# Kernel optimization log

Hardware: AMD Instinct MI355X
Metric: run time of the kernel (lower is better)

Reference implementation:

```python
import jax, jax.numpy as jnp
import numpy as np

TOP_K = 2
NUM_EXPERTS = 64
LOAD_BALANCE_ALPHA = 0.01
Z_LOSS_ALPHA = 1e-4
TEMPERATURE = 1.0  # buffer init, clamped to [0.1, 2.0] -> 1.0 (seq_len < 8192 branch)


def setup_inputs() -> dict:
    key = jax.random.key(0)
    k1, k2 = jax.random.split(key)
    x = jax.random.normal(k1, (4, 4096, 1024), dtype=jnp.float32)
    gate_w = jax.random.normal(k2, (NUM_EXPERTS, 1024), dtype=jnp.float32) * (1.0 / np.sqrt(1024))
    return {"x": x, "gate_w": gate_w}


def reference(x, gate_w):
    B, S, H = x.shape
    x_flat = x.reshape(-1, H)                      # [T, H], T = B*S
    logits = jnp.einsum('th,eh->te', x_flat, gate_w)  # [T, E]
    logits = logits / TEMPERATURE
    scores = jax.nn.softmax(logits, axis=-1)       # [T, E]
    # eval path: dynamic_top_k == top_k, no noise / capacity limitation
    top_scores, top_idx = jax.lax.top_k(scores, TOP_K)   # [T, K]
    top_scores = jax.nn.softmax(top_scores.astype(jnp.float32), axis=-1).astype(x.dtype)
    # load-balance loss: squared deviation of mean expert load from uniform
    expert_load = scores.mean(axis=0)              # [E]
    ideal = 1.0 / NUM_EXPERTS
    lb_loss = LOAD_BALANCE_ALPHA * NUM_EXPERTS * jnp.sum((expert_load - ideal) ** 2)
    # z-loss: mean squared logsumexp of gate logits
    z = jax.nn.logsumexp(logits, axis=-1)          # [T]
    z_loss = Z_LOSS_ALPHA * jnp.mean(z ** 2)
    total_loss = lb_loss + z_loss
    return top_scores, top_idx, total_loss
```

## Files before the change

kernel.cpp:

```cpp
#include <hip/hip_runtime.h>
#include <math.h>

#define T_TOK 16384
#define NEXP  64


__global__ void moe_prep(const float* __restrict__ gw, float* __restrict__ ws) {
    __shared__ float tile[64][65];
    const int b = blockIdx.x;
    const int tid = threadIdx.x;
    if (b == 0 && tid < 128) ws[tid] = 0.f;
#pragma unroll
    for (int it = 0; it < 16; ++it) {
        int idx = it * 256 + tid;
        int e = idx >> 6, kk = idx & 63;
        tile[e][kk] = gw[e * 1024 + b * 64 + kk];
    }
    __syncthreads();
#pragma unroll
    for (int it = 0; it < 16; ++it) {
        int idx = it * 256 + tid;
        int kk = idx >> 6, e = idx & 63;
        ws[128 + (b * 64 + kk) * 64 + e] = tile[e][kk];
    }
}

__device__ __forceinline__ void pstore(float* B, const float (&a)[8][8],
                                       int tg, int eg) {
#pragma unroll
    for (int i = 0; i < 8; ++i) {
        float* p = B + (tg + 8 * i) * 68 + (eg << 3);
        *(float4*)(p)     = make_float4(a[i][0], a[i][1], a[i][2], a[i][3]);
        *(float4*)(p + 4) = make_float4(a[i][4], a[i][5], a[i][6], a[i][7]);
    }
}
__device__ __forceinline__ void padd(float* B, const float (&a)[8][8],
                                     int tg, int eg) {
#pragma unroll
    for (int i = 0; i < 8; ++i) {
        float* p = B + (tg + 8 * i) * 68 + (eg << 3);
        float4 v0 = *(float4*)(p);
        float4 v1 = *(float4*)(p + 4);
        v0.x += a[i][0]; v0.y += a[i][1]; v0.z += a[i][2]; v0.w += a[i][3];
        v1.x += a[i][4]; v1.y += a[i][5]; v1.z += a[i][6]; v1.w += a[i][7];
        *(float4*)(p)     = v0;
        *(float4*)(p + 4) = v1;
    }
}

__launch_bounds__(1024, 4)
__global__ void moe_main(const float* __restrict__ x,
                         const float* __restrict__ wt,
                         float* __restrict__ acc_ws,
                         float* __restrict__ out) {
    __shared__ float xbuf[64 * 68];
    __shared__ float wbuf[64 * 68];
    __shared__ float sc[64 * 68];
    __shared__ float row_inv[64];
    __shared__ float colpart[16][64];
    __shared__ int   is_last;

    const int tid  = threadIdx.x;
    const int lane = tid & 63;
    const int wv   = __builtin_amdgcn_readfirstlane(tid >> 6);
    const int tg   = lane & 7;
    const int eg   = lane >> 3;
    const int tok0 = blockIdx.x << 6;

    const int rr = tid >> 4;
    const int cg = tid & 15;
    const float* gx = x + (((size_t)(tok0 + rr)) << 10) + (cg << 2);
    const float* gw = wt + (rr << 6) + (cg << 2);
    const int lof = rr * 68 + (cg << 2);

    float acc[8][8];
#pragma unroll
    for (int i = 0; i < 8; ++i)
#pragma unroll
        for (int j = 0; j < 8; ++j) acc[i][j] = 0.f;

    const float* xr = xbuf + tg * 68 + (wv << 2);
    const float* wr = wbuf + (wv * 4) * 68 + (eg << 3);

    float4 px = *(const float4*)gx;
    float4 pw = *(const float4*)gw;

#pragma unroll 1
    for (int s = 0; s < 16; ++s) {
        __syncthreads();
        *(float4*)(xbuf + lof) = px;
        *(float4*)(wbuf + lof) = pw;
        __syncthreads();
        if (s < 15) {
            px = *(const float4*)(gx + ((s + 1) << 6));
            pw = *(const float4*)(gw + ((s + 1) << 12));
        }
        float wa[4][8];
#pragma unroll
        for (int u = 0; u < 4; ++u) {
            float4 q0 = *(const float4*)(wr + u * 68);
            float4 q1 = *(const float4*)(wr + u * 68 + 4);
            wa[u][0] = q0.x; wa[u][1] = q0.y; wa[u][2] = q0.z; wa[u][3] = q0.w;
            wa[u][4] = q1.x; wa[u][5] = q1.y; wa[u][6] = q1.z; wa[u][7] = q1.w;
        }
#pragma unroll
        for (int i = 0; i < 8; ++i) {
            float4 xc = *(const float4*)(xr + i * 544);
            float xa[4] = {xc.x, xc.y, xc.z, xc.w};
#pragma unroll
            for (int u = 0; u < 4; ++u) {
                float xv = xa[u];
#pragma unroll
                for (int j = 0; j < 8; ++j)
                    acc[i][j] = fmaf(xv, wa[u][j], acc[i][j]);
            }
        }
    }

    __syncthreads();
    if      (wv == 0) pstore(sc,   acc, tg, eg);
    else if (wv == 1) pstore(xbuf, acc, tg, eg);
    else if (wv == 2) pstore(wbuf, acc, tg, eg);
    __syncthreads();
    if      (wv == 3) padd(sc,   acc, tg, eg);
    else if (wv == 4) padd(xbuf, acc, tg, eg);
    else if (wv == 5) padd(wbuf, acc, tg, eg);
    __syncthreads();
    if      (wv == 6) padd(sc,   acc, tg, eg);
    else if (wv == 7) padd(xbuf, acc, tg, eg);
    else if (wv == 8) padd(wbuf, acc, tg, eg);
    __syncthreads();
    if      (wv == 9)  padd(sc,   acc, tg, eg);
    else if (wv == 10) padd(xbuf, acc, tg, eg);
    else if (wv == 11) padd(wbuf, acc, tg, eg);
    __syncthreads();
    if      (wv == 12) padd(sc,   acc, tg, eg);
    else if (wv == 13) padd(xbuf, acc, tg, eg);
    else if (wv == 14) padd(wbuf, acc, tg, eg);
    __syncthreads();
    if (wv == 15) padd(sc, acc, tg, eg);
    __syncthreads();
    {
        const int row = tid >> 4, g = tid & 15;
        float* ps = sc + row * 68 + (g << 2);
        float4 a  = *(float4*)ps;
        float4 bx = *(const float4*)(xbuf + row * 68 + (g << 2));
        float4 bw = *(const float4*)(wbuf + row * 68 + (g << 2));
        a.x += bx.x + bw.x; a.y += bx.y + bw.y;
        a.z += bx.z + bw.z; a.w += bx.w + bw.w;
        *(float4*)ps = a;
    }
    __syncthreads();

    if (tid < 64) {
        const int r = tid;
        const float* srow = sc + r * 68;
        float v1 = -1e30f, v2 = -1e30f;
        int i1 = 0, i2 = 0;
        for (int j = 0; j < 64; ++j) {
            float l = srow[j];
            if (l > v1)      { v2 = v1; i2 = i1; v1 = l; i1 = j; }
            else if (l > v2) { v2 = l; i2 = j; }
        }
        float m = v1;
        float ssum = 0.f;
        for (int j = 0; j < 64; ++j) {
            float ev = expf(srow[j] - m);
            ssum += ev;
            sc[r * 68 + j] = ev;
        }
        float inv = 1.f / ssum;
        row_inv[r] = inv;
        float z = m + logf(ssum);
        float zsq = z * z;
#pragma unroll
        for (int off = 32; off > 0; off >>= 1) zsq += __shfl_down(zsq, off);
        if (lane == 0) atomicAdd(acc_ws + 64, zsq);

        float p1s = inv;
        float p2s = expf(v2 - m) * inv;
        float bb  = expf(p2s - p1s);
        float s1 = 1.f / (1.f + bb);
        float s2 = bb * s1;
        int t = tok0 + r;
        out[2 * t]     = s1;
        out[2 * t + 1] = s2;
        out[2 * T_TOK + 2 * t]     = (float)i1;
        out[2 * T_TOK + 2 * t + 1] = (float)i2;
    }
    __syncthreads();

    {
        int e  = tid & 63;
        int rg = tid >> 6;
        float sum = 0.f;
#pragma unroll
        for (int r2 = 0; r2 < 4; ++r2) {
            int row = (rg << 2) + r2;
            sum += sc[row * 68 + e] * row_inv[row];
        }
        colpart[rg][e] = sum;
    }
    __syncthreads();
    if (tid < 64) {
        float tot = 0.f;
#pragma unroll
        for (int rg = 0; rg < 16; ++rg) tot += colpart[rg][tid];
        atomicAdd(acc_ws + tid, tot);
    }

    __syncthreads();
    if (tid == 0) {
        __threadfence();
        int old = __hip_atomic_fetch_add((int*)(acc_ws + 66), 1,
                                         __ATOMIC_ACQ_REL, __HIP_MEMORY_SCOPE_AGENT);
        is_last = (old == 255) ? 1 : 0;
    }
    __syncthreads();
    if (is_last && tid < 64) {
        __threadfence();
        float load = __hip_atomic_load(acc_ws + tid, __ATOMIC_RELAXED,
                                       __HIP_MEMORY_SCOPE_AGENT) * (1.f / 16384.f);
        float d = load - (1.f / 64.f);
        float v = d * d;
#pragma unroll
        for (int off = 32; off > 0; off >>= 1) v += __shfl_down(v, off);
        if (tid == 0) {
            float zsum = __hip_atomic_load(acc_ws + 64, __ATOMIC_RELAXED,
                                           __HIP_MEMORY_SCOPE_AGENT);
            float lb = 0.01f * 64.f * v;
            float zl = 1e-4f * zsum * (1.f / 16384.f);
            out[4 * T_TOK] = lb + zl;
        }
    }
}

extern "C" void kernel_launch(void* const* d_in, const int* in_sizes, int n_in,
                              void* d_out, int out_size, void* d_ws, size_t ws_size,
                              hipStream_t stream) {
    const float* x  = (const float*)d_in[0];
    const float* gw = (const float*)d_in[1];
    float* out = (float*)d_out;
    float* ws  = (float*)d_ws;

    moe_prep<<<16, 256, 0, stream>>>(gw, ws);
    moe_main<<<256, 1024, 0, stream>>>(x, ws + 128, ws, out);
}
```

Before: 131.0 us.

## Double-buffer x tile with XOR swizzle; read gate weights directly from global

The x tile is now double-buffered in LDS with an XOR-swizzled layout, so each K-step needs one barrier instead of two and the next tile is stored while the current one is consumed. Gate weights skip the LDS staging entirely: each thread loads its 4x8 weight slice straight from global (L2-resident transposed weights) each step. This cuts LDS traffic and barriers, but adds redundant global weight loads across waves and blocks, and their latency is exposed within the step.

```diff
diff --git a/kernel.cpp b/kernel.cpp
--- a/kernel.cpp
+++ b/kernel.cpp
@@ -53,8 +53,7 @@
                          const float* __restrict__ wt,
                          float* __restrict__ acc_ws,
                          float* __restrict__ out) {
-    __shared__ float xbuf[64 * 68];
-    __shared__ float wbuf[64 * 68];
+    __shared__ float xs[2 * 4352];
     __shared__ float sc[64 * 68];
     __shared__ float row_inv[64];
     __shared__ float colpart[16][64];
@@ -67,11 +66,14 @@
     const int eg   = lane >> 3;
     const int tok0 = blockIdx.x << 6;
 
-    const int rr = tid >> 4;
-    const int cg = tid & 15;
-    const float* gx = x + (((size_t)(tok0 + rr)) << 10) + (cg << 2);
-    const float* gw = wt + (rr << 6) + (cg << 2);
-    const int lof = rr * 68 + (cg << 2);
+    const int srow = tid >> 4;
+    const int sgs  = tid & 15;
+    const float* gx = x + (((size_t)(tok0 + srow)) << 10) + ((sgs ^ (srow & 7)) << 2);
+    const int wloc = (srow << 6) + (sgs << 2);
+
+    const float* gw0 = wt + (wv << 8) + (eg << 3);
+
+    const int xoff = (tg << 6) + ((wv ^ tg) << 2);
 
     float acc[8][8];
 #pragma unroll
@@ -79,33 +81,36 @@
 #pragma unroll
         for (int j = 0; j < 8; ++j) acc[i][j] = 0.f;
 
-    const float* xr = xbuf + tg * 68 + (wv << 2);
-    const float* wr = wbuf + (wv * 4) * 68 + (eg << 3);
-
     float4 px = *(const float4*)gx;
-    float4 pw = *(const float4*)gw;
-
+    *(float4*)(xs + wloc) = px;
+    px = *(const float4*)(gx + 64);
+    __syncthreads();
+
+    int rb = 0;
 #pragma unroll 1
     for (int s = 0; s < 16; ++s) {
-        __syncthreads();
-        *(float4*)(xbuf + lof) = px;
-        *(float4*)(wbuf + lof) = pw;
-        __syncthreads();
+        const float* gwr = gw0 + (s << 12);
+        float4 w0a = *(const float4*)(gwr);
+        float4 w0b = *(const float4*)(gwr + 4);
+        float4 w1a = *(const float4*)(gwr + 64);
+        float4 w1b = *(const float4*)(gwr + 68);
+        float4 w2a = *(const float4*)(gwr + 128);
+        float4 w2b = *(const float4*)(gwr + 132);
+        float4 w3a = *(const float4*)(gwr + 192);
+        float4 w3b = *(const float4*)(gwr + 196);
         if (s < 15) {
-            px = *(const float4*)(gx + ((s + 1) << 6));
-            pw = *(const float4*)(gw + ((s + 1) << 12));
-        }
-        float wa[4][8];
-#pragma unroll
-        for (int u = 0; u < 4; ++u) {
-            float4 q0 = *(const float4*)(wr + u * 68);
-            float4 q1 = *(const float4*)(wr + u * 68 + 4);
-            wa[u][0] = q0.x; wa[u][1] = q0.y; wa[u][2] = q0.z; wa[u][3] = q0.w;
-            wa[u][4] = q1.x; wa[u][5] = q1.y; wa[u][6] = q1.z; wa[u][7] = q1.w;
-        }
+            *(float4*)(xs + (rb ^ 4352) + wloc) = px;
+            if (s < 14) px = *(const float4*)(gx + ((s + 2) << 6));
+        }
+        const float wa[4][8] = {
+            {w0a.x, w0a.y, w0a.z, w0a.w, w0b.x, w0b.y, w0b.z, w0b.w},
+            {w1a.x, w1a.y, w1a.z, w1a.w, w1b.x, w1b.y, w1b.z, w1b.w},
+            {w2a.x, w2a.y, w2a.z, w2a.w, w2b.x, w2b.y, w2b.z, w2b.w},
+            {w3a.x, w3a.y, w3a.z, w3a.w, w3b.x, w3b.y, w3b.z, w3b.w}};
+        const float* rdp = xs + rb + xoff;
 #pragma unroll
         for (int i = 0; i < 8; ++i) {
-            float4 xc = *(const float4*)(xr + i * 544);
+            float4 xc = *(const float4*)(rdp + (i << 9));
             float xa[4] = {xc.x, xc.y, xc.z, xc.w};
 #pragma unroll
             for (int u = 0; u < 4; ++u) {
@@ -115,28 +120,31 @@
                     acc[i][j] = fmaf(xv, wa[u][j], acc[i][j]);
             }
         }
-    }
-
-    __syncthreads();
-    if      (wv == 0) pstore(sc,   acc, tg, eg);
-    else if (wv == 1) pstore(xbuf, acc, tg, eg);
-    else if (wv == 2) pstore(wbuf, acc, tg, eg);
-    __syncthreads();
-    if      (wv == 3) padd(sc,   acc, tg, eg);
-    else if (wv == 4) padd(xbuf, acc, tg, eg);
-    else if (wv == 5) padd(wbuf, acc, tg, eg);
-    __syncthreads();
-    if      (wv == 6) padd(sc,   acc, tg, eg);
-    else if (wv == 7) padd(xbuf, acc, tg, eg);
-    else if (wv == 8) padd(wbuf, acc, tg, eg);
-    __syncthreads();
-    if      (wv == 9)  padd(sc,   acc, tg, eg);
-    else if (wv == 10) padd(xbuf, acc, tg, eg);
-    else if (wv == 11) padd(wbuf, acc, tg, eg);
-    __syncthreads();
-    if      (wv == 12) padd(sc,   acc, tg, eg);
-    else if (wv == 13) padd(xbuf, acc, tg, eg);
-    else if (wv == 14) padd(wbuf, acc, tg, eg);
+        __syncthreads();
+        rb ^= 4352;
+    }
+
+    float* fb0 = xs;
+    float* fb1 = xs + 4352;
+    if      (wv == 0) pstore(sc,  acc, tg, eg);
+    else if (wv == 1) pstore(fb0, acc, tg, eg);
+    else if (wv == 2) pstore(fb1, acc, tg, eg);
+    __syncthreads();
+    if      (wv == 3) padd(sc,  acc, tg, eg);
+    else if (wv == 4) padd(fb0, acc, tg, eg);
+    else if (wv == 5) padd(fb1, acc, tg, eg);
+    __syncthreads();
+    if      (wv == 6) padd(sc,  acc, tg, eg);
+    else if (wv == 7) padd(fb0, acc, tg, eg);
+    else if (wv == 8) padd(fb1, acc, tg, eg);
+    __syncthreads();
+    if      (wv == 9)  padd(sc,  acc, tg, eg);
+    else if (wv == 10) padd(fb0, acc, tg, eg);
+    else if (wv == 11) padd(fb1, acc, tg, eg);
+    __syncthreads();
+    if      (wv == 12) padd(sc,  acc, tg, eg);
+    else if (wv == 13) padd(fb0, acc, tg, eg);
+    else if (wv == 14) padd(fb1, acc, tg, eg);
     __syncthreads();
     if (wv == 15) padd(sc, acc, tg, eg);
     __syncthreads();
@@ -144,8 +152,8 @@
         const int row = tid >> 4, g = tid & 15;
         float* ps = sc + row * 68 + (g << 2);
         float4 a  = *(float4*)ps;
-        float4 bx = *(const float4*)(xbuf + row * 68 + (g << 2));
-        float4 bw = *(const float4*)(wbuf + row * 68 + (g << 2));
+        float4 bx = *(const float4*)(fb0 + row * 68 + (g << 2));
+        float4 bw = *(const float4*)(fb1 + row * 68 + (g << 2));
         a.x += bx.x + bw.x; a.y += bx.y + bw.y;
         a.z += bx.z + bw.z; a.w += bx.w + bw.w;
         *(float4*)ps = a;
@@ -154,18 +162,18 @@
 
     if (tid < 64) {
         const int r = tid;
-        const float* srow = sc + r * 68;
+        const float* srow_p = sc + r * 68;
         float v1 = -1e30f, v2 = -1e30f;
         int i1 = 0, i2 = 0;
         for (int j = 0; j < 64; ++j) {
-            float l = srow[j];
+            float l = srow_p[j];
             if (l > v1)      { v2 = v1; i2 = i1; v1 = l; i1 = j; }
             else if (l > v2) { v2 = l; i2 = j; }
         }
         float m = v1;
         float ssum = 0.f;
         for (int j = 0; j < 64; ++j) {
-            float ev = expf(srow[j] - m);
+            float ev = expf(srow_p[j] - m);
             ssum += ev;
             sc[r * 68 + j] = ev;
         }
```

Measured after the change: 135.3 us. 1.03x slower.

## Halve token tile, double-buffer LDS, split K across half-waves with shuffle reduce

Applied to the files above, without the earlier changes.

Each block now handles 32 tokens with 512 threads, so 512 blocks are launched instead of 256. The x and gate-weight tiles are double-buffered in shared memory, which drops one barrier per K step. Within each wave the two half-waves take different K halves, and their partial sums are combined with a cross-lane shuffle before the shared-memory reduction. The aim is better occupancy across CUs and less barrier stall, at the cost of reloading the full weight tile per block, which doubles weight traffic.

```diff
diff --git a/kernel.cpp b/kernel.cpp
--- a/kernel.cpp
+++ b/kernel.cpp
@@ -25,20 +25,22 @@
     }
 }
 
-__device__ __forceinline__ void pstore(float* B, const float (&a)[8][8],
-                                       int tg, int eg) {
-#pragma unroll
-    for (int i = 0; i < 8; ++i) {
-        float* p = B + (tg + 8 * i) * 68 + (eg << 3);
+__device__ __forceinline__ void pstore4(float* B, const float (&a)[8][8],
+                                        int tg, int eg, int i0) {
+#pragma unroll
+    for (int ii = 0; ii < 4; ++ii) {
+        int i = i0 + ii;
+        float* p = B + (tg + 4 * i) * 68 + (eg << 3);
         *(float4*)(p)     = make_float4(a[i][0], a[i][1], a[i][2], a[i][3]);
         *(float4*)(p + 4) = make_float4(a[i][4], a[i][5], a[i][6], a[i][7]);
     }
 }
-__device__ __forceinline__ void padd(float* B, const float (&a)[8][8],
-                                     int tg, int eg) {
-#pragma unroll
-    for (int i = 0; i < 8; ++i) {
-        float* p = B + (tg + 8 * i) * 68 + (eg << 3);
+__device__ __forceinline__ void padd4(float* B, const float (&a)[8][8],
+                                      int tg, int eg, int i0) {
+#pragma unroll
+    for (int ii = 0; ii < 4; ++ii) {
+        int i = i0 + ii;
+        float* p = B + (tg + 4 * i) * 68 + (eg << 3);
         float4 v0 = *(float4*)(p);
         float4 v1 = *(float4*)(p + 4);
         v0.x += a[i][0]; v0.y += a[i][1]; v0.z += a[i][2]; v0.w += a[i][3];
@@ -48,30 +50,33 @@
     }
 }
 
-__launch_bounds__(1024, 4)
+__launch_bounds__(512, 4)
 __global__ void moe_main(const float* __restrict__ x,
                          const float* __restrict__ wt,
                          float* __restrict__ acc_ws,
                          float* __restrict__ out) {
-    __shared__ float xbuf[64 * 68];
-    __shared__ float wbuf[64 * 68];
-    __shared__ float sc[64 * 68];
-    __shared__ float row_inv[64];
-    __shared__ float colpart[16][64];
+    __shared__ float xs[2 * 2176];
+    __shared__ float wl[2 * 4352];
+    __shared__ float sc[32 * 68];
+    __shared__ float row_inv[32];
+    __shared__ float colpart[8][64];
     __shared__ int   is_last;
 
     const int tid  = threadIdx.x;
     const int lane = tid & 63;
     const int wv   = __builtin_amdgcn_readfirstlane(tid >> 6);
-    const int tg   = lane & 7;
-    const int eg   = lane >> 3;
-    const int tok0 = blockIdx.x << 6;
-
-    const int rr = tid >> 4;
-    const int cg = tid & 15;
-    const float* gx = x + (((size_t)(tok0 + rr)) << 10) + (cg << 2);
-    const float* gw = wt + (rr << 6) + (cg << 2);
-    const int lof = rr * 68 + (cg << 2);
+    const int tg   = lane & 3;
+    const int eg   = (lane >> 2) & 7;
+    const int kh   = lane >> 5;
+    const int tok0 = blockIdx.x << 5;
+
+    const int srow = tid >> 4;
+    const int sg   = tid & 15;
+    const float* gx = x + (((size_t)(tok0 + srow)) << 10) + (sg << 2);
+    const int xwloc = srow * 68 + (sg << 2);
+    const float* gw = wt + (srow << 6) + (sg << 2);
+    const int wwloc  = srow * 68 + (sg << 2);
+    const int wwloc2 = (srow + 32) * 68 + (sg << 2);
 
     float acc[8][8];
 #pragma unroll
@@ -79,22 +84,34 @@
 #pragma unroll
         for (int j = 0; j < 8; ++j) acc[i][j] = 0.f;
 
-    const float* xr = xbuf + tg * 68 + (wv << 2);
-    const float* wr = wbuf + (wv * 4) * 68 + (eg << 3);
-
-    float4 px = *(const float4*)gx;
-    float4 pw = *(const float4*)gw;
-
+    const int kcol = (kh << 5) + (wv << 2);
+    const int xoff = tg * 68 + kcol;
+    const int woff = kcol * 68 + (eg << 3);
+
+    *(float4*)(xs + xwloc)  = *(const float4*)gx;
+    *(float4*)(wl + wwloc)  = *(const float4*)gw;
+    *(float4*)(wl + wwloc2) = *(const float4*)(gw + 2048);
+    float4 px  = *(const float4*)(gx + 64);
+    float4 pw0 = *(const float4*)(gw + 4096);
+    float4 pw1 = *(const float4*)(gw + 4096 + 2048);
+    __syncthreads();
+
+    int p = 0;
 #pragma unroll 1
     for (int s = 0; s < 16; ++s) {
-        __syncthreads();
-        *(float4*)(xbuf + lof) = px;
-        *(float4*)(wbuf + lof) = pw;
-        __syncthreads();
         if (s < 15) {
-            px = *(const float4*)(gx + ((s + 1) << 6));
-            pw = *(const float4*)(gw + ((s + 1) << 12));
-        }
+            const int q = p ^ 1;
+            *(float4*)(xs + q * 2176 + xwloc)  = px;
+            *(float4*)(wl + q * 4352 + wwloc)  = pw0;
+            *(float4*)(wl + q * 4352 + wwloc2) = pw1;
+            if (s < 14) {
+                px  = *(const float4*)(gx + ((s + 2) << 6));
+                pw0 = *(const float4*)(gw + ((s + 2) << 12));
+                pw1 = *(const float4*)(gw + ((s + 2) << 12) + 2048);
+            }
+        }
+        const float* xr = xs + p * 2176 + xoff;
+        const float* wr = wl + p * 4352 + woff;
         float wa[4][8];
 #pragma unroll
         for (int u = 0; u < 4; ++u) {
@@ -105,7 +122,7 @@
         }
 #pragma unroll
         for (int i = 0; i < 8; ++i) {
-            float4 xc = *(const float4*)(xr + i * 544);
+            float4 xc = *(const float4*)(xr + i * 272);
             float xa[4] = {xc.x, xc.y, xc.z, xc.w};
 #pragma unroll
             for (int u = 0; u < 4; ++u) {
@@ -115,57 +132,56 @@
                     acc[i][j] = fmaf(xv, wa[u][j], acc[i][j]);
             }
         }
-    }
-
-    __syncthreads();
-    if      (wv == 0) pstore(sc,   acc, tg, eg);
-    else if (wv == 1) pstore(xbuf, acc, tg, eg);
-    else if (wv == 2) pstore(wbuf, acc, tg, eg);
-    __syncthreads();
-    if      (wv == 3) padd(sc,   acc, tg, eg);
-    else if (wv == 4) padd(xbuf, acc, tg, eg);
-    else if (wv == 5) padd(wbuf, acc, tg, eg);
-    __syncthreads();
-    if      (wv == 6) padd(sc,   acc, tg, eg);
-    else if (wv == 7) padd(xbuf, acc, tg, eg);
-    else if (wv == 8) padd(wbuf, acc, tg, eg);
-    __syncthreads();
-    if      (wv == 9)  padd(sc,   acc, tg, eg);
-    else if (wv == 10) padd(xbuf, acc, tg, eg);
-    else if (wv == 11) padd(wbuf, acc, tg, eg);
-    __syncthreads();
-    if      (wv == 12) padd(sc,   acc, tg, eg);
-    else if (wv == 13) padd(xbuf, acc, tg, eg);
-    else if (wv == 14) padd(wbuf, acc, tg, eg);
-    __syncthreads();
-    if (wv == 15) padd(sc, acc, tg, eg);
+        __syncthreads();
+        p ^= 1;
+    }
+
+#pragma unroll
+    for (int i = 0; i < 8; ++i)
+#pragma unroll
+        for (int j = 0; j < 8; ++j)
+            acc[i][j] += __shfl_xor(acc[i][j], 32);
+
+    const int i0 = kh << 2;
+    float* fb0 = xs;
+    float* fb1 = xs + 2176;
+    if      (wv == 0) pstore4(sc,  acc, tg, eg, i0);
+    else if (wv == 1) pstore4(fb0, acc, tg, eg, i0);
+    else if (wv == 2) pstore4(fb1, acc, tg, eg, i0);
+    __syncthreads();
+    if      (wv == 3) padd4(sc,  acc, tg, eg, i0);
+    else if (wv == 4) padd4(fb0, acc, tg, eg, i0);
+    else if (wv == 5) padd4(fb1, acc, tg, eg, i0);
+    __syncthreads();
+    if      (wv == 6) padd4(sc,  acc, tg, eg, i0);
+    else if (wv == 7) padd4(fb0, acc, tg, eg, i0);
     __syncthreads();
     {
         const int row = tid >> 4, g = tid & 15;
         float* ps = sc + row * 68 + (g << 2);
         float4 a  = *(float4*)ps;
-        float4 bx = *(const float4*)(xbuf + row * 68 + (g << 2));
-        float4 bw = *(const float4*)(wbuf + row * 68 + (g << 2));
+        float4 bx = *(const float4*)(fb0 + row * 68 + (g << 2));
+        float4 bw = *(const float4*)(fb1 + row * 68 + (g << 2));
         a.x += bx.x + bw.x; a.y += bx.y + bw.y;
         a.z += bx.z + bw.z; a.w += bx.w + bw.w;
         *(float4*)ps = a;
     }
     __syncthreads();
 
-    if (tid < 64) {
+    if (tid < 32) {
         const int r = tid;
-        const float* srow = sc + r * 68;
+        const float* srow_p = sc + r * 68;
         float v1 = -1e30f, v2 = -1e30f;
         int i1 = 0, i2 = 0;
         for (int j = 0; j < 64; ++j) {
-            float l = srow[j];
+            float l = srow_p[j];
             if (l > v1)      { v2 = v1; i2 = i1; v1 = l; i1 = j; }
             else if (l > v2) { v2 = l; i2 = j; }
         }
         float m = v1;
         float ssum = 0.f;
         for (int j = 0; j < 64; ++j) {
-            float ev = expf(srow[j] - m);
+            float ev = expf(srow_p[j] - m);
             ssum += ev;
             sc[r * 68 + j] = ev;
         }
@@ -174,8 +190,8 @@
         float z = m + logf(ssum);
         float zsq = z * z;
 #pragma unroll
-        for (int off = 32; off > 0; off >>= 1) zsq += __shfl_down(zsq, off);
-        if (lane == 0) atomicAdd(acc_ws + 64, zsq);
+        for (int off = 16; off > 0; off >>= 1) zsq += __shfl_down(zsq, off);
+        if (tid == 0) atomicAdd(acc_ws + 64, zsq);
 
         float p1s = inv;
         float p2s = expf(v2 - m) * inv;
@@ -205,7 +221,7 @@
     if (tid < 64) {
         float tot = 0.f;
 #pragma unroll
-        for (int rg = 0; rg < 16; ++rg) tot += colpart[rg][tid];
+        for (int rg = 0; rg < 8; ++rg) tot += colpart[rg][tid];
         atomicAdd(acc_ws + tid, tot);
     }
 
@@ -214,7 +230,7 @@
         __threadfence();
         int old = __hip_atomic_fetch_add((int*)(acc_ws + 66), 1,
                                          __ATOMIC_ACQ_REL, __HIP_MEMORY_SCOPE_AGENT);
-        is_last = (old == 255) ? 1 : 0;
+        is_last = (old == 511) ? 1 : 0;
     }
     __syncthreads();
     if (is_last && tid < 64) {
@@ -244,5 +260,5 @@
     float* ws  = (float*)d_ws;
 
     moe_prep<<<16, 256, 0, stream>>>(gw, ws);
-    moe_main<<<256, 1024, 0, stream>>>(x, ws + 128, ws, out);
-}
+    moe_main<<<512, 512, 0, stream>>>(x, ws + 128, ws, out);
+}
```

After: 368.6 us. +181.4%, slower.

## Split GEMM tile into 4x8 per-thread blocks with 8-way K split and XOR-swizzled x tile

Applied to the files above, without the earlier changes.

Restructures the in-block logits GEMM so each wave owns half the tokens and one eighth of the K slice. Each thread accumulates a 4x8 tile instead of 8x8, which halves accumulator registers, and the launch bound changes from 4 to 1 blocks per CU. The x tile is now stored unpadded with an XOR swizzle to avoid LDS bank conflicts, and a separate buffer cuts the cross-wave reduction to fewer barrier rounds. The trade-off is more LDS reads per FMA and a different occupancy profile.

```diff
diff --git a/kernel.cpp b/kernel.cpp
--- a/kernel.cpp
+++ b/kernel.cpp
@@ -25,20 +25,20 @@
     }
 }
 
-__device__ __forceinline__ void pstore(float* B, const float (&a)[8][8],
-                                       int tg, int eg) {
-#pragma unroll
-    for (int i = 0; i < 8; ++i) {
-        float* p = B + (tg + 8 * i) * 68 + (eg << 3);
+__device__ __forceinline__ void pst8(float* B, const float (&a)[4][8],
+                                     int t0, int eb) {
+#pragma unroll
+    for (int i = 0; i < 4; ++i) {
+        float* p = B + (t0 + i) * 68 + (eb << 3);
         *(float4*)(p)     = make_float4(a[i][0], a[i][1], a[i][2], a[i][3]);
         *(float4*)(p + 4) = make_float4(a[i][4], a[i][5], a[i][6], a[i][7]);
     }
 }
-__device__ __forceinline__ void padd(float* B, const float (&a)[8][8],
-                                     int tg, int eg) {
-#pragma unroll
-    for (int i = 0; i < 8; ++i) {
-        float* p = B + (tg + 8 * i) * 68 + (eg << 3);
+__device__ __forceinline__ void pad8(float* B, const float (&a)[4][8],
+                                     int t0, int eb) {
+#pragma unroll
+    for (int i = 0; i < 4; ++i) {
+        float* p = B + (t0 + i) * 68 + (eb << 3);
         float4 v0 = *(float4*)(p);
         float4 v1 = *(float4*)(p + 4);
         v0.x += a[i][0]; v0.y += a[i][1]; v0.z += a[i][2]; v0.w += a[i][3];
@@ -48,39 +48,45 @@
     }
 }
 
-__launch_bounds__(1024, 4)
+__launch_bounds__(1024, 1)
 __global__ void moe_main(const float* __restrict__ x,
                          const float* __restrict__ wt,
                          float* __restrict__ acc_ws,
                          float* __restrict__ out) {
-    __shared__ float xbuf[64 * 68];
-    __shared__ float wbuf[64 * 68];
+    __shared__ float xbuf[64 * 64];
+    __shared__ float wbuf[64 * 64];
     __shared__ float sc[64 * 68];
+    __shared__ float fb[64 * 68];
     __shared__ float row_inv[64];
     __shared__ float colpart[16][64];
     __shared__ int   is_last;
 
     const int tid  = threadIdx.x;
     const int lane = tid & 63;
-    const int wv   = __builtin_amdgcn_readfirstlane(tid >> 6);
-    const int tg   = lane & 7;
-    const int eg   = lane >> 3;
+    const int wv   = tid >> 6;
+    const int kq   = __builtin_amdgcn_readfirstlane(wv & 7);
+    const int tt   = __builtin_amdgcn_readfirstlane(wv >> 3);
+    const int ta = lane >> 3;
+    const int eb = lane & 7;
     const int tok0 = blockIdx.x << 6;
 
     const int rr = tid >> 4;
     const int cg = tid & 15;
     const float* gx = x + (((size_t)(tok0 + rr)) << 10) + (cg << 2);
+    const int rm2s = ((rr & 3) << 2) | ((rr >> 2) & 3);
+    const int xlo = (rr << 6) + ((cg ^ rm2s) << 2);
     const float* gw = wt + (rr << 6) + (cg << 2);
-    const int lof = rr * 68 + (cg << 2);
-
-    float acc[8][8];
-#pragma unroll
-    for (int i = 0; i < 8; ++i)
+    const int wlo = (rr << 6) + (cg << 2);
+
+    float acc[4][8];
+#pragma unroll
+    for (int i = 0; i < 4; ++i)
 #pragma unroll
         for (int j = 0; j < 8; ++j) acc[i][j] = 0.f;
 
-    const float* xr = xbuf + tg * 68 + (wv << 2);
-    const float* wr = wbuf + (wv * 4) * 68 + (eg << 3);
+    const int t0 = (tt << 5) + (ta << 2);
+    const int rhi = (t0 >> 2) & 3;
+    const int ebase = eb << 3;
 
     float4 px = *(const float4*)gx;
     float4 pw = *(const float4*)gw;
@@ -88,66 +94,68 @@
 #pragma unroll 1
     for (int s = 0; s < 16; ++s) {
         __syncthreads();
-        *(float4*)(xbuf + lof) = px;
-        *(float4*)(wbuf + lof) = pw;
+        *(float4*)(xbuf + xlo) = px;
+        *(float4*)(wbuf + wlo) = pw;
         __syncthreads();
         if (s < 15) {
             px = *(const float4*)(gx + ((s + 1) << 6));
             pw = *(const float4*)(gw + ((s + 1) << 12));
         }
-        float wa[4][8];
-#pragma unroll
-        for (int u = 0; u < 4; ++u) {
-            float4 q0 = *(const float4*)(wr + u * 68);
-            float4 q1 = *(const float4*)(wr + u * 68 + 4);
-            wa[u][0] = q0.x; wa[u][1] = q0.y; wa[u][2] = q0.z; wa[u][3] = q0.w;
-            wa[u][4] = q1.x; wa[u][5] = q1.y; wa[u][6] = q1.z; wa[u][7] = q1.w;
-        }
-#pragma unroll
-        for (int i = 0; i < 8; ++i) {
-            float4 xc = *(const float4*)(xr + i * 544);
-            float xa[4] = {xc.x, xc.y, xc.z, xc.w};
-#pragma unroll
-            for (int u = 0; u < 4; ++u) {
-                float xv = xa[u];
-#pragma unroll
-                for (int j = 0; j < 8; ++j)
-                    acc[i][j] = fmaf(xv, wa[u][j], acc[i][j]);
+#pragma unroll
+        for (int kp = 0; kp < 4; ++kp) {
+            const int c   = (kq << 1) + (kp >> 1);
+            const int sub = kp & 1;
+            float2 xf0, xf1, xf2, xf3;
+            {
+                const int b0 = ((t0 + 0) << 6) + ((c ^ ((0 << 2) | rhi)) << 2) + (sub << 1);
+                const int b1 = ((t0 + 1) << 6) + ((c ^ ((1 << 2) | rhi)) << 2) + (sub << 1);
+                const int b2 = ((t0 + 2) << 6) + ((c ^ ((2 << 2) | rhi)) << 2) + (sub << 1);
+                const int b3 = ((t0 + 3) << 6) + ((c ^ ((3 << 2) | rhi)) << 2) + (sub << 1);
+                xf0 = *(const float2*)(xbuf + b0);
+                xf1 = *(const float2*)(xbuf + b1);
+                xf2 = *(const float2*)(xbuf + b2);
+                xf3 = *(const float2*)(xbuf + b3);
             }
-        }
-    }
-
-    __syncthreads();
-    if      (wv == 0) pstore(sc,   acc, tg, eg);
-    else if (wv == 1) pstore(xbuf, acc, tg, eg);
-    else if (wv == 2) pstore(wbuf, acc, tg, eg);
-    __syncthreads();
-    if      (wv == 3) padd(sc,   acc, tg, eg);
-    else if (wv == 4) padd(xbuf, acc, tg, eg);
-    else if (wv == 5) padd(wbuf, acc, tg, eg);
-    __syncthreads();
-    if      (wv == 6) padd(sc,   acc, tg, eg);
-    else if (wv == 7) padd(xbuf, acc, tg, eg);
-    else if (wv == 8) padd(wbuf, acc, tg, eg);
-    __syncthreads();
-    if      (wv == 9)  padd(sc,   acc, tg, eg);
-    else if (wv == 10) padd(xbuf, acc, tg, eg);
-    else if (wv == 11) padd(wbuf, acc, tg, eg);
-    __syncthreads();
-    if      (wv == 12) padd(sc,   acc, tg, eg);
-    else if (wv == 13) padd(xbuf, acc, tg, eg);
-    else if (wv == 14) padd(wbuf, acc, tg, eg);
-    __syncthreads();
-    if (wv == 15) padd(sc, acc, tg, eg);
+#pragma unroll
+            for (int h = 0; h < 2; ++h) {
+                const int rk = (kq << 3) + (kp << 1) + h;
+                const float* wr = wbuf + (rk << 6) + ebase;
+                float4 w0 = *(const float4*)(wr);
+                float4 w1 = *(const float4*)(wr + 4);
+                float wa[8] = {w0.x, w0.y, w0.z, w0.w, w1.x, w1.y, w1.z, w1.w};
+                float xv0 = h ? xf0.y : xf0.x;
+                float xv1 = h ? xf1.y : xf1.x;
+                float xv2 = h ? xf2.y : xf2.x;
+                float xv3 = h ? xf3.y : xf3.x;
+#pragma unroll
+                for (int j = 0; j < 8; ++j) {
+                    acc[0][j] = fmaf(xv0, wa[j], acc[0][j]);
+                    acc[1][j] = fmaf(xv1, wa[j], acc[1][j]);
+                    acc[2][j] = fmaf(xv2, wa[j], acc[2][j]);
+                    acc[3][j] = fmaf(xv3, wa[j], acc[3][j]);
+                }
+            }
+        }
+    }
+
+    if      (kq == 0) pst8(sc, acc, t0, eb);
+    else if (kq == 1) pst8(fb, acc, t0, eb);
+    __syncthreads();
+    if      (kq == 2) pad8(sc, acc, t0, eb);
+    else if (kq == 3) pad8(fb, acc, t0, eb);
+    __syncthreads();
+    if      (kq == 4) pad8(sc, acc, t0, eb);
+    else if (kq == 5) pad8(fb, acc, t0, eb);
+    __syncthreads();
+    if      (kq == 6) pad8(sc, acc, t0, eb);
+    else if (kq == 7) pad8(fb, acc, t0, eb);
     __syncthreads();
     {
         const int row = tid >> 4, g = tid & 15;
         float* ps = sc + row * 68 + (g << 2);
         float4 a  = *(float4*)ps;
-        float4 bx = *(const float4*)(xbuf + row * 68 + (g << 2));
-        float4 bw = *(const float4*)(wbuf + row * 68 + (g << 2));
-        a.x += bx.x + bw.x; a.y += bx.y + bw.y;
-        a.z += bx.z + bw.z; a.w += bx.w + bw.w;
+        float4 bx = *(const float4*)(fb + row * 68 + (g << 2));
+        a.x += bx.x; a.y += bx.y; a.z += bx.z; a.w += bx.w;
         *(float4*)ps = a;
     }
     __syncthreads();
```

Result: no change. 128.7 us (-1.8%).
